# Kernel tuning notes

Hardware: AMD Instinct MI355X
Metric: run time of the kernel (lower is better)

## Reference

```python
import jax, jax.numpy as jnp
import numpy as np

N = 100000
E = 3200000
F_IN, HID, C = 256, 128, 40


def setup_inputs() -> dict:
    key = jax.random.key(0)
    k1, k2, k3, k4, k5 = jax.random.split(key, 5)
    x = jax.random.normal(k1, (N, F_IN), dtype=jnp.float32)
    edge_index = jax.random.randint(k2, (2, E), 0, N, dtype=jnp.int64)
    edge_weight = jax.random.uniform(k3, (E,), dtype=jnp.float32)
    W1 = jax.random.normal(k4, (F_IN, HID), dtype=jnp.float32) * (1.0 / np.sqrt(F_IN))
    b1 = jnp.zeros((HID,), dtype=jnp.float32)
    W2 = jax.random.normal(k5, (HID, C), dtype=jnp.float32) * (1.0 / np.sqrt(HID))
    b2 = jnp.zeros((C,), dtype=jnp.float32)
    return {"x": x, "edge_index": edge_index, "edge_weight": edge_weight,
            "W1": W1, "b1": b1, "W2": W2, "b2": b2}


def gcn_conv(x, edge_index, edge_weight, W, b):
    # PyG GCNConv (add_self_loops=False, normalize=False):
    # 1) linear transform, 2) edge-weighted scatter-add from src to dst.
    h = x @ W  # [N, d_out]
    src, dst = edge_index[0], edge_index[1]
    msgs = h[src] * edge_weight[:, None]  # [E, d_out]
    agg = jax.ops.segment_sum(msgs, dst, num_segments=x.shape[0])
    return agg + b


def reference(x, edge_index, edge_weight, W1, b1, W2, b2):
    # dropout is identity in eval mode
    h = jax.nn.relu(gcn_conv(x, edge_index, edge_weight, W1, b1))
    out = gcn_conv(h, edge_index, edge_weight, W2, b2)
    return jax.nn.log_softmax(out, axis=1)
```

## Files before the change

kernel.cpp:

```cpp
#include <hip/hip_runtime.h>
#include <hip/hip_bf16.h>
#include <hip/hip_fp16.h>
#include <math.h>

#define N_NODES 100000
#define E_EDGES 3200000
#define F_INF   256
#define HIDF    128
#define C_OUT   40

#define BSH   8
#define NB    391
#define NSEG  32
#define CAP   384
#define OCAP  262144
#define EPB   1563
#define SCAT_BLOCKS 2048
#define W1T_BLOCKS  128
#define GEMM1_BLOCKS ((N_NODES + 127) / 128)

typedef __attribute__((ext_vector_type(8))) short bf16x8;
typedef __attribute__((ext_vector_type(4))) float f32x4;

static __device__ __forceinline__ short bf16c(float f) {
    __hip_bfloat16 b = __float2bfloat16(f);
    return *reinterpret_cast<short*>(&b);
}

static __device__ void scat_body(int bid, const int* __restrict__ ei,
        const float* __restrict__ ew, int* __restrict__ cnt,
        int2* __restrict__ rec, int* __restrict__ ocnt,
        int2* __restrict__ osw, int* __restrict__ odst) {
    int seg = bid & (NSEG - 1);
    int e0 = bid * EPB;
    int e1 = e0 + EPB; if (e1 > E_EDGES) e1 = E_EDGES;
    for (int e = e0 + threadIdx.x; e < e1; e += 256) {
        int dst = ei[E_EDGES + e];
        int src = ei[e];
        float w = ew[e];
        int b = dst >> BSH;
        int packed = src | ((dst & 255) << 17);
        int pos = atomicAdd(&cnt[seg * NB + b], 1);
        if (pos < CAP) {
            rec[(size_t)(seg * NB + b) * CAP + pos] =
                make_int2(packed, __float_as_int(w));
        } else {
            int op = atomicAdd(ocnt, 1);
            if (op < OCAP) { osw[op] = make_int2(src, __float_as_int(w)); odst[op] = dst; }
        }
    }
}

static __device__ void w1t_body(int bid, const float* __restrict__ W1,
                                short* __restrict__ w1t) {
    int idx = bid * 256 + threadIdx.x;
    int k = idx >> 7, c = idx & 127;
    w1t[c * 256 + k] = bf16c(W1[idx]);
}

__global__ __launch_bounds__(256) void scat_w1t_kernel(const int* __restrict__ ei,
        const float* __restrict__ ew, int* __restrict__ cnt,
        int2* __restrict__ rec, int* __restrict__ ocnt,
        int2* __restrict__ osw, int* __restrict__ odst,
        const float* __restrict__ W1, short* __restrict__ w1t) {
    if (blockIdx.x < SCAT_BLOCKS)
        scat_body(blockIdx.x, ei, ew, cnt, rec, ocnt, osw, odst);
    else
        w1t_body(blockIdx.x - SCAT_BLOCKS, W1, w1t);
}

static __device__ void csr_body(char* smem, int b, const int* __restrict__ cnt,
        const int2* __restrict__ rec, const int* __restrict__ ocnt,
        const int2* __restrict__ osw, const int* __restrict__ odst,
        int* __restrict__ rowptr, int2* __restrict__ srcw) {
    int* hist = (int*)smem;
    int* sc   = hist + 256;
    int* cur  = sc + 256;
    int* red  = cur + 256;
    int* s_base = red + 4;
    int tid = threadIdx.x;
    hist[tid] = 0;

    int partial = 0;
    for (int i = tid; i < b * NSEG; i += 256) {
        int bp = i >> 5, s = i & 31;
        int c = cnt[s * NB + bp];
        partial += (c < CAP ? c : CAP);
    }
    int onum = *ocnt; if (onum > OCAP) onum = OCAP;
    for (int i = tid; i < onum; i += 256)
        if ((odst[i] >> BSH) < b) ++partial;
    #pragma unroll
    for (int off = 32; off; off >>= 1) partial += __shfl_xor(partial, off);
    if ((tid & 63) == 0) red[tid >> 6] = partial;
    __syncthreads();
    if (tid == 0) *s_base = red[0] + red[1] + red[2] + red[3];
    __syncthreads();

    for (int s = 0; s < NSEG; ++s) {
        int c = cnt[s * NB + b]; if (c > CAP) c = CAP;
        const int2* rp = &rec[(size_t)(s * NB + b) * CAP];
        for (int i = tid; i < c; i += 256)
            atomicAdd(&hist[(rp[i].x >> 17) & 255], 1);
    }
    for (int i = tid; i < onum; i += 256) {
        int d = odst[i];
        if ((d >> BSH) == b) atomicAdd(&hist[d & 255], 1);
    }
    __syncthreads();

    sc[tid] = hist[tid];
    __syncthreads();
    for (int off = 1; off < 256; off <<= 1) {
        int v = (tid >= off) ? sc[tid - off] : 0;
        __syncthreads();
        sc[tid] += v;
        __syncthreads();
    }
    int excl = (tid > 0) ? sc[tid - 1] : 0;
    cur[tid] = excl;
    int base = *s_base;
    int node = b * 256 + tid;
    if (node <= N_NODES) rowptr[node] = base + excl;
    __syncthreads();

    for (int s = 0; s < NSEG; ++s) {
        int c = cnt[s * NB + b]; if (c > CAP) c = CAP;
        const int2* rp = &rec[(size_t)(s * NB + b) * CAP];
        for (int i = tid; i < c; i += 256) {
            int2 r = rp[i];
            int dl = (r.x >> 17) & 255;
            int p = atomicAdd(&cur[dl], 1);
            srcw[base + p] = make_int2(r.x & 0x1FFFF, r.y);
        }
    }
    for (int i = tid; i < onum; i += 256) {
        int d = odst[i];
        if ((d >> BSH) == b) {
            int p = atomicAdd(&cur[d & 255], 1);
            srcw[base + p] = osw[i];
        }
    }
}

static __device__ void gemm1_body(char* smem, int bid, const float* __restrict__ x,
                                  const short* __restrict__ w1t,
                                  __half* __restrict__ h) {
    short* aT = (short*)smem;
    int tid = threadIdx.x;
    int lane = tid & 63, wid = tid >> 6;
    int wr = wid >> 1, wc = wid & 1;
    int m0 = bid * 128;
    f32x4 acc[4][4] = {{{0.f}}};
    for (int kb = 0; kb < 256; kb += 64) {
        #pragma unroll
        for (int t = 0; t < 8; ++t) {
            int id = tid + t * 256;
            int row = id >> 4, c4 = id & 15;
            int gr = m0 + row; if (gr >= N_NODES) gr = N_NODES - 1;
            float4 g = *(const float4*)&x[(size_t)gr * F_INF + kb + c4 * 4];
            short4 s4 = { bf16c(g.x), bf16c(g.y), bf16c(g.z), bf16c(g.w) };
            int byte = row * 128 + c4 * 8;
            byte ^= (row & 7) << 4;
            *(short4*)(smem + byte) = s4;
        }
        __syncthreads();
        #pragma unroll
        for (int km = 0; km < 2; ++km) {
            bf16x8 af[4], bfr[4];
            #pragma unroll
            for (int mi = 0; mi < 4; ++mi) {
                int row = wr * 64 + mi * 16 + (lane & 15);
                int kk = km * 32 + (lane >> 4) * 8;
                int byte = row * 128 + kk * 2;
                byte ^= (row & 7) << 4;
                af[mi] = *(bf16x8*)(smem + byte);
            }
            #pragma unroll
            for (int ni = 0; ni < 4; ++ni) {
                int col = wc * 64 + ni * 16 + (lane & 15);
                int kk = kb + km * 32 + (lane >> 4) * 8;
                bfr[ni] = *(const bf16x8*)&w1t[col * 256 + kk];
            }
            #pragma unroll
            for (int mi = 0; mi < 4; ++mi)
                #pragma unroll
                for (int ni = 0; ni < 4; ++ni)
                    acc[mi][ni] = __builtin_amdgcn_mfma_f32_16x16x32_bf16(
                        af[mi], bfr[ni], acc[mi][ni], 0, 0, 0);
        }
        __syncthreads();
    }
    #pragma unroll
    for (int mi = 0; mi < 4; ++mi) {
        int rbase = m0 + wr * 64 + mi * 16 + ((lane >> 4) << 2);
        #pragma unroll
        for (int ni = 0; ni < 4; ++ni) {
            int col = wc * 64 + ni * 16 + (lane & 15);
            #pragma unroll
            for (int r = 0; r < 4; ++r) {
                int row = rbase + r;
                if (row < N_NODES)
                    h[(size_t)row * HIDF + col] = __float2half(acc[mi][ni][r]);
            }
        }
    }
}

__global__ __launch_bounds__(256) void csr_gemm1_kernel(const int* __restrict__ cnt,
        const int2* __restrict__ rec, const int* __restrict__ ocnt,
        const int2* __restrict__ osw, const int* __restrict__ odst,
        int* __restrict__ rowptr, int2* __restrict__ srcw,
        const float* __restrict__ x, const short* __restrict__ w1t,
        __half* __restrict__ h) {
    __shared__ char smem[16384];
    if (blockIdx.x < NB)
        csr_body(smem, blockIdx.x, cnt, rec, ocnt, osw, odst, rowptr, srcw);
    else
        gemm1_body(smem, blockIdx.x - NB, x, w1t, h);
}

__global__ __launch_bounds__(256) void agg1_kernel(const __half* __restrict__ h,
                                                   const int2* __restrict__ srcw,
                                                   const int* __restrict__ rowptr,
                                                   const float* __restrict__ b1,
                                                   __half* __restrict__ hact) {
    int lane = threadIdx.x & 63;
    int node = blockIdx.x * 4 + (threadIdx.x >> 6);
    if (node >= N_NODES) return;
    int beg = rowptr[node], end = rowptr[node + 1];
    int eo = lane >> 4, fo = lane & 15;
    float4 a0 = {0.f, 0.f, 0.f, 0.f}, a1 = {0.f, 0.f, 0.f, 0.f};
    const uint4* hp = (const uint4*)h;
    for (int base = beg; base < end; base += 64) {
        int idx = base + lane;
        int2 sw = srcw[idx < end ? idx : end - 1];
        int cnt = end - base; if (cnt > 64) cnt = 64;
        for (int j = 0; j < cnt; j += 8) {
            int jj0 = j + eo, jj1 = j + 4 + eo;
            int s0 = __shfl(sw.x, jj0);
            float w0 = __int_as_float(__shfl(sw.y, jj0));
            int s1 = __shfl(sw.x, jj1);
            float w1 = __int_as_float(__shfl(sw.y, jj1));
            if (jj0 >= cnt) w0 = 0.f;
            if (jj1 >= cnt) w1 = 0.f;
            uint4 hv0 = hp[(size_t)s0 * 16 + fo];
            uint4 hv1 = hp[(size_t)s1 * 16 + fo];
            const __half2* p0 = (const __half2*)&hv0;
            const __half2* p1 = (const __half2*)&hv1;
            float2 f;
            f = __half22float2(p0[0]); a0.x += w0 * f.x; a0.y += w0 * f.y;
            f = __half22float2(p0[1]); a0.z += w0 * f.x; a0.w += w0 * f.y;
            f = __half22float2(p0[2]); a1.x += w0 * f.x; a1.y += w0 * f.y;
            f = __half22float2(p0[3]); a1.z += w0 * f.x; a1.w += w0 * f.y;
            f = __half22float2(p1[0]); a0.x += w1 * f.x; a0.y += w1 * f.y;
            f = __half22float2(p1[1]); a0.z += w1 * f.x; a0.w += w1 * f.y;
            f = __half22float2(p1[2]); a1.x += w1 * f.x; a1.y += w1 * f.y;
            f = __half22float2(p1[3]); a1.z += w1 * f.x; a1.w += w1 * f.y;
        }
    }
    #pragma unroll
    for (int off = 16; off < 64; off <<= 1) {
        a0.x += __shfl_xor(a0.x, off); a0.y += __shfl_xor(a0.y, off);
        a0.z += __shfl_xor(a0.z, off); a0.w += __shfl_xor(a0.w, off);
        a1.x += __shfl_xor(a1.x, off); a1.y += __shfl_xor(a1.y, off);
        a1.z += __shfl_xor(a1.z, off); a1.w += __shfl_xor(a1.w, off);
    }
    if (lane < 16) {
        float4 bb0 = *(const float4*)&b1[fo * 8];
        float4 bb1 = *(const float4*)&b1[fo * 8 + 4];
        __half2 o0 = __floats2half2_rn(fmaxf(a0.x + bb0.x, 0.f), fmaxf(a0.y + bb0.y, 0.f));
        __half2 o1 = __floats2half2_rn(fmaxf(a0.z + bb0.z, 0.f), fmaxf(a0.w + bb0.w, 0.f));
        __half2 o2 = __floats2half2_rn(fmaxf(a1.x + bb1.x, 0.f), fmaxf(a1.y + bb1.y, 0.f));
        __half2 o3 = __floats2half2_rn(fmaxf(a1.z + bb1.z, 0.f), fmaxf(a1.w + bb1.w, 0.f));
        uint4 ov = { *(uint*)&o0, *(uint*)&o1, *(uint*)&o2, *(uint*)&o3 };
        ((uint4*)hact)[(size_t)node * 16 + fo] = ov;
    }
}

__global__ __launch_bounds__(320) void gemm2_kernel(const __half* __restrict__ hact,
                                                    const float* __restrict__ W2,
                                                    __half* __restrict__ h2) {
    __shared__ float xT[128 * 68];
    __shared__ float w2[128 * 40];
    int tid = threadIdx.x;
    int tx = tid % 40, ty = tid / 40;
    int m0 = blockIdx.x * 64;
    for (int i = tid; i < 128 * 40; i += 320) w2[i] = W2[i];
    for (int i = tid; i < 1024; i += 320) {
        int row = i >> 4, c8 = i & 15;
        int gr = m0 + row; if (gr >= N_NODES) gr = N_NODES - 1;
        uint4 v = *(const uint4*)&hact[(size_t)gr * HIDF + c8 * 8];
        const __half2* ph = (const __half2*)&v;
        #pragma unroll
        for (int t = 0; t < 4; ++t) {
            float2 f = __half22float2(ph[t]);
            int k = c8 * 8 + t * 2;
            xT[(k + 0) * 68 + row] = f.x;
            xT[(k + 1) * 68 + row] = f.y;
        }
    }
    __syncthreads();
    float acc[8] = {};
    #pragma unroll 4
    for (int k = 0; k < 128; ++k) {
        float wv = w2[k * 40 + tx];
        float4 xa = *(float4*)&xT[k * 68 + ty * 8];
        float4 xb = *(float4*)&xT[k * 68 + ty * 8 + 4];
        acc[0] += xa.x * wv; acc[1] += xa.y * wv;
        acc[2] += xa.z * wv; acc[3] += xa.w * wv;
        acc[4] += xb.x * wv; acc[5] += xb.y * wv;
        acc[6] += xb.z * wv; acc[7] += xb.w * wv;
    }
    #pragma unroll
    for (int i = 0; i < 8; ++i) {
        int r = m0 + ty * 8 + i;
        if (r < N_NODES) h2[(size_t)r * C_OUT + tx] = __float2half(acc[i]);
    }
}

__global__ __launch_bounds__(256) void agg2_kernel(const __half* __restrict__ h2,
                                                   const int2* __restrict__ srcw,
                                                   const int* __restrict__ rowptr,
                                                   const float* __restrict__ b2,
                                                   float* __restrict__ out) {
    int lane = threadIdx.x & 63;
    int node = blockIdx.x * 4 + (threadIdx.x >> 6);
    if (node >= N_NODES) return;
    int beg = rowptr[node], end = rowptr[node + 1];
    int eo = lane >> 4, fo = lane & 15;
    float4 acc = {0.f, 0.f, 0.f, 0.f};
    const uint2* hp = (const uint2*)h2;
    for (int base = beg; base < end; base += 64) {
        int idx = base + lane;
        int2 sw = srcw[idx < end ? idx : end - 1];
        int cnt = end - base; if (cnt > 64) cnt = 64;
        for (int j = 0; j < cnt; j += 8) {
            int jj0 = j + eo, jj1 = j + 4 + eo;
            int s0 = __shfl(sw.x, jj0);
            float w0 = __int_as_float(__shfl(sw.y, jj0));
            int s1 = __shfl(sw.x, jj1);
            float w1 = __int_as_float(__shfl(sw.y, jj1));
            if (jj0 >= cnt) w0 = 0.f;
            if (jj1 >= cnt) w1 = 0.f;
            if (fo < 10) {
                uint2 hv0 = hp[(size_t)s0 * 10 + fo];
                uint2 hv1 = hp[(size_t)s1 * 10 + fo];
                float2 f;
                f = __half22float2(*(__half2*)&hv0.x); acc.x += w0 * f.x; acc.y += w0 * f.y;
                f = __half22float2(*(__half2*)&hv0.y); acc.z += w0 * f.x; acc.w += w0 * f.y;
                f = __half22float2(*(__half2*)&hv1.x); acc.x += w1 * f.x; acc.y += w1 * f.y;
                f = __half22float2(*(__half2*)&hv1.y); acc.z += w1 * f.x; acc.w += w1 * f.y;
            }
        }
    }
    #pragma unroll
    for (int off = 16; off < 64; off <<= 1) {
        acc.x += __shfl_xor(acc.x, off); acc.y += __shfl_xor(acc.y, off);
        acc.z += __shfl_xor(acc.z, off); acc.w += __shfl_xor(acc.w, off);
    }
    float4 v = {-INFINITY, -INFINITY, -INFINITY, -INFINITY};
    if (fo < 10) {
        float4 bb = *(const float4*)&b2[fo * 4];
        v.x = acc.x + bb.x; v.y = acc.y + bb.y;
        v.z = acc.z + bb.z; v.w = acc.w + bb.w;
    }
    float m = fmaxf(fmaxf(v.x, v.y), fmaxf(v.z, v.w));
    #pragma unroll
    for (int off = 8; off; off >>= 1) m = fmaxf(m, __shfl_xor(m, off));
    float ex = 0.f;
    if (fo < 10)
        ex = expf(v.x - m) + expf(v.y - m) + expf(v.z - m) + expf(v.w - m);
    #pragma unroll
    for (int off = 8; off; off >>= 1) ex += __shfl_xor(ex, off);
    float ls = logf(ex);
    if (lane < 16 && fo < 10) {
        float4 o = { v.x - m - ls, v.y - m - ls, v.z - m - ls, v.w - m - ls };
        *(float4*)&out[(size_t)node * C_OUT + fo * 4] = o;
    }
}


extern "C" void kernel_launch(void* const* d_in, const int* in_sizes, int n_in,
                              void* d_out, int out_size, void* d_ws, size_t ws_size,
                              hipStream_t stream) {
    const float* x  = (const float*)d_in[0];
    const int*   ei = (const int*)d_in[1];
    const float* ew = (const float*)d_in[2];
    const float* W1 = (const float*)d_in[3];
    const float* b1 = (const float*)d_in[4];
    const float* W2 = (const float*)d_in[5];
    const float* b2 = (const float*)d_in[6];
    float* out = (float*)d_out;

    char* ws = (char*)d_ws;
    size_t off = 0;
    auto alloc = [&](size_t bytes) -> void* {
        void* p = ws + off;
        off += (bytes + 255) & ~(size_t)255;
        return p;
    };
    __half* h      = (__half*)alloc((size_t)N_NODES * HIDF * 2);
    __half* hact   = (__half*)alloc((size_t)N_NODES * HIDF * 2);
    __half* h2     = (__half*)alloc((size_t)N_NODES * C_OUT * 2);
    short*  w1t    = (short*)alloc((size_t)HIDF * F_INF * 2);
    int*    rowptr = (int*)alloc((size_t)(N_NODES + 1) * 4);
    int2*   srcw   = (int2*)alloc((size_t)E_EDGES * 8);
    int2*   rec    = (int2*)alloc((size_t)NSEG * NB * CAP * 8);
    int*    cnt    = (int*)alloc((size_t)NSEG * NB * 4);
    int*    ocnt   = (int*)alloc(256);
    int2*   osw    = (int2*)alloc((size_t)OCAP * 8);
    int*    odst   = (int*)alloc((size_t)OCAP * 4);

    hipMemsetAsync(cnt, 0, (size_t)NSEG * NB * 4, stream);
    hipMemsetAsync(ocnt, 0, 4, stream);

    scat_w1t_kernel<<<SCAT_BLOCKS + W1T_BLOCKS, 256, 0, stream>>>(
        ei, ew, cnt, rec, ocnt, osw, odst, W1, w1t);
    csr_gemm1_kernel<<<NB + GEMM1_BLOCKS, 256, 0, stream>>>(
        cnt, rec, ocnt, osw, odst, rowptr, srcw, x, w1t, h);
    agg1_kernel<<<(N_NODES + 3) / 4, 256, 0, stream>>>(h, srcw, rowptr, b1, hact);
    gemm2_kernel<<<(N_NODES + 63) / 64, 320, 0, stream>>>(hact, W2, h2);
    agg2_kernel<<<(N_NODES + 3) / 4, 256, 0, stream>>>(h2, srcw, rowptr, b2, out);
}
```

Before: 559.5 us.

## Pad h2 to 64 halves and widen gather loads, prefetch edge lists

The layer-2 features are stored padded to 64 halfs per row (zero-filled tail) so agg2 can gather 16-byte rows with 8 lanes per edge and 8 edges in flight, replacing 8-byte loads with 10 of 16 lanes active. Both aggregation kernels now prefetch the next 64-edge chunk of src/weight records and issue four (agg1) or two (agg2) independent row gathers per iteration to raise memory-level parallelism. The padding adds extra h2 write and read traffic per row, and the larger unroll raises register pressure.

```diff
diff --git a/kernel.cpp b/kernel.cpp
--- a/kernel.cpp
+++ b/kernel.cpp
@@ -8,6 +8,7 @@
 #define F_INF   256
 #define HIDF    128
 #define C_OUT   40
+#define H2P     64
 
 #define BSH   8
 #define NB    391
@@ -146,7 +147,6 @@
 static __device__ void gemm1_body(char* smem, int bid, const float* __restrict__ x,
                                   const short* __restrict__ w1t,
                                   __half* __restrict__ h) {
-    short* aT = (short*)smem;
     int tid = threadIdx.x;
     int lane = tid & 63, wid = tid >> 6;
     int wr = wid >> 1, wc = wid & 1;
@@ -232,32 +232,35 @@
     int eo = lane >> 4, fo = lane & 15;
     float4 a0 = {0.f, 0.f, 0.f, 0.f}, a1 = {0.f, 0.f, 0.f, 0.f};
     const uint4* hp = (const uint4*)h;
+    int idx0 = beg + lane;
+    int2 sw = srcw[idx0 < end ? idx0 : end - 1];
     for (int base = beg; base < end; base += 64) {
-        int idx = base + lane;
-        int2 sw = srcw[idx < end ? idx : end - 1];
         int cnt = end - base; if (cnt > 64) cnt = 64;
-        for (int j = 0; j < cnt; j += 8) {
-            int jj0 = j + eo, jj1 = j + 4 + eo;
-            int s0 = __shfl(sw.x, jj0);
-            float w0 = __int_as_float(__shfl(sw.y, jj0));
-            int s1 = __shfl(sw.x, jj1);
-            float w1 = __int_as_float(__shfl(sw.y, jj1));
-            if (jj0 >= cnt) w0 = 0.f;
-            if (jj1 >= cnt) w1 = 0.f;
-            uint4 hv0 = hp[(size_t)s0 * 16 + fo];
-            uint4 hv1 = hp[(size_t)s1 * 16 + fo];
-            const __half2* p0 = (const __half2*)&hv0;
-            const __half2* p1 = (const __half2*)&hv1;
-            float2 f;
-            f = __half22float2(p0[0]); a0.x += w0 * f.x; a0.y += w0 * f.y;
-            f = __half22float2(p0[1]); a0.z += w0 * f.x; a0.w += w0 * f.y;
-            f = __half22float2(p0[2]); a1.x += w0 * f.x; a1.y += w0 * f.y;
-            f = __half22float2(p0[3]); a1.z += w0 * f.x; a1.w += w0 * f.y;
-            f = __half22float2(p1[0]); a0.x += w1 * f.x; a0.y += w1 * f.y;
-            f = __half22float2(p1[1]); a0.z += w1 * f.x; a0.w += w1 * f.y;
-            f = __half22float2(p1[2]); a1.x += w1 * f.x; a1.y += w1 * f.y;
-            f = __half22float2(p1[3]); a1.z += w1 * f.x; a1.w += w1 * f.y;
-        }
+        int nidx = base + 64 + lane;
+        int2 swn = srcw[nidx < end ? nidx : end - 1];
+        for (int j = 0; j < cnt; j += 16) {
+            int s[4]; float w[4];
+            #pragma unroll
+            for (int u = 0; u < 4; ++u) {
+                int jj = j + u * 4 + eo;
+                s[u] = __shfl(sw.x, jj);
+                w[u] = __int_as_float(__shfl(sw.y, jj));
+                if (jj >= cnt) w[u] = 0.f;
+            }
+            uint4 hv[4];
+            #pragma unroll
+            for (int u = 0; u < 4; ++u) hv[u] = hp[(size_t)s[u] * 16 + fo];
+            #pragma unroll
+            for (int u = 0; u < 4; ++u) {
+                const __half2* p = (const __half2*)&hv[u];
+                float2 f;
+                f = __half22float2(p[0]); a0.x += w[u] * f.x; a0.y += w[u] * f.y;
+                f = __half22float2(p[1]); a0.z += w[u] * f.x; a0.w += w[u] * f.y;
+                f = __half22float2(p[2]); a1.x += w[u] * f.x; a1.y += w[u] * f.y;
+                f = __half22float2(p[3]); a1.z += w[u] * f.x; a1.w += w[u] * f.y;
+            }
+        }
+        sw = swn;
     }
     #pragma unroll
     for (int off = 16; off < 64; off <<= 1) {
@@ -280,7 +283,7 @@
 
 __global__ __launch_bounds__(320) void gemm2_kernel(const __half* __restrict__ hact,
                                                     const float* __restrict__ W2,
-                                                    __half* __restrict__ h2) {
+                                                    __half* __restrict__ h2p) {
     __shared__ float xT[128 * 68];
     __shared__ float w2[128 * 40];
     int tid = threadIdx.x;
@@ -300,6 +303,14 @@
             xT[(k + 1) * 68 + row] = f.y;
         }
     }
+    for (int i = tid; i < 64 * 3; i += 320) {
+        int row = i / 3, c = i % 3;
+        int gr = m0 + row;
+        if (gr < N_NODES) {
+            uint4 z = {0, 0, 0, 0};
+            *(uint4*)&h2p[(size_t)gr * H2P + 40 + c * 8] = z;
+        }
+    }
     __syncthreads();
     float acc[8] = {};
     #pragma unroll 4
@@ -315,11 +326,11 @@
     #pragma unroll
     for (int i = 0; i < 8; ++i) {
         int r = m0 + ty * 8 + i;
-        if (r < N_NODES) h2[(size_t)r * C_OUT + tx] = __float2half(acc[i]);
-    }
-}
-
-__global__ __launch_bounds__(256) void agg2_kernel(const __half* __restrict__ h2,
+        if (r < N_NODES) h2p[(size_t)r * H2P + tx] = __float2half(acc[i]);
+    }
+}
+
+__global__ __launch_bounds__(256) void agg2_kernel(const __half* __restrict__ h2p,
                                                    const int2* __restrict__ srcw,
                                                    const int* __restrict__ rowptr,
                                                    const float* __restrict__ b2,
@@ -328,55 +339,76 @@
     int node = blockIdx.x * 4 + (threadIdx.x >> 6);
     if (node >= N_NODES) return;
     int beg = rowptr[node], end = rowptr[node + 1];
-    int eo = lane >> 4, fo = lane & 15;
-    float4 acc = {0.f, 0.f, 0.f, 0.f};
-    const uint2* hp = (const uint2*)h2;
+    int eo = lane >> 3, fo = lane & 7;
+    float4 a0 = {0.f, 0.f, 0.f, 0.f}, a1 = {0.f, 0.f, 0.f, 0.f};
+    const uint4* hp = (const uint4*)h2p;
+    int idx0 = beg + lane;
+    int2 sw = srcw[idx0 < end ? idx0 : end - 1];
     for (int base = beg; base < end; base += 64) {
-        int idx = base + lane;
-        int2 sw = srcw[idx < end ? idx : end - 1];
         int cnt = end - base; if (cnt > 64) cnt = 64;
-        for (int j = 0; j < cnt; j += 8) {
-            int jj0 = j + eo, jj1 = j + 4 + eo;
-            int s0 = __shfl(sw.x, jj0);
-            float w0 = __int_as_float(__shfl(sw.y, jj0));
-            int s1 = __shfl(sw.x, jj1);
-            float w1 = __int_as_float(__shfl(sw.y, jj1));
-            if (jj0 >= cnt) w0 = 0.f;
-            if (jj1 >= cnt) w1 = 0.f;
-            if (fo < 10) {
-                uint2 hv0 = hp[(size_t)s0 * 10 + fo];
-                uint2 hv1 = hp[(size_t)s1 * 10 + fo];
+        int nidx = base + 64 + lane;
+        int2 swn = srcw[nidx < end ? nidx : end - 1];
+        for (int j = 0; j < cnt; j += 16) {
+            int s[2]; float w[2];
+            #pragma unroll
+            for (int u = 0; u < 2; ++u) {
+                int jj = j + u * 8 + eo;
+                s[u] = __shfl(sw.x, jj);
+                w[u] = __int_as_float(__shfl(sw.y, jj));
+                if (jj >= cnt) w[u] = 0.f;
+            }
+            uint4 hv[2];
+            #pragma unroll
+            for (int u = 0; u < 2; ++u) hv[u] = hp[(size_t)s[u] * 8 + fo];
+            #pragma unroll
+            for (int u = 0; u < 2; ++u) {
+                const __half2* p = (const __half2*)&hv[u];
                 float2 f;
-                f = __half22float2(*(__half2*)&hv0.x); acc.x += w0 * f.x; acc.y += w0 * f.y;
-                f = __half22float2(*(__half2*)&hv0.y); acc.z += w0 * f.x; acc.w += w0 * f.y;
-                f = __half22float2(*(__half2*)&hv1.x); acc.x += w1 * f.x; acc.y += w1 * f.y;
-                f = __half22float2(*(__half2*)&hv1.y); acc.z += w1 * f.x; acc.w += w1 * f.y;
-            }
-        }
-    }
-    #pragma unroll
-    for (int off = 16; off < 64; off <<= 1) {
-        acc.x += __shfl_xor(acc.x, off); acc.y += __shfl_xor(acc.y, off);
-        acc.z += __shfl_xor(acc.z, off); acc.w += __shfl_xor(acc.w, off);
-    }
-    float4 v = {-INFINITY, -INFINITY, -INFINITY, -INFINITY};
-    if (fo < 10) {
-        float4 bb = *(const float4*)&b2[fo * 4];
-        v.x = acc.x + bb.x; v.y = acc.y + bb.y;
-        v.z = acc.z + bb.z; v.w = acc.w + bb.w;
-    }
-    float m = fmaxf(fmaxf(v.x, v.y), fmaxf(v.z, v.w));
-    #pragma unroll
-    for (int off = 8; off; off >>= 1) m = fmaxf(m, __shfl_xor(m, off));
+                f = __half22float2(p[0]); a0.x += w[u] * f.x; a0.y += w[u] * f.y;
+                f = __half22float2(p[1]); a0.z += w[u] * f.x; a0.w += w[u] * f.y;
+                f = __half22float2(p[2]); a1.x += w[u] * f.x; a1.y += w[u] * f.y;
+                f = __half22float2(p[3]); a1.z += w[u] * f.x; a1.w += w[u] * f.y;
+            }
+        }
+        sw = swn;
+    }
+    #pragma unroll
+    for (int off = 8; off < 64; off <<= 1) {
+        a0.x += __shfl_xor(a0.x, off); a0.y += __shfl_xor(a0.y, off);
+        a0.z += __shfl_xor(a0.z, off); a0.w += __shfl_xor(a0.w, off);
+        a1.x += __shfl_xor(a1.x, off); a1.y += __shfl_xor(a1.y, off);
+        a1.z += __shfl_xor(a1.z, off); a1.w += __shfl_xor(a1.w, off);
+    }
+    float v[8];
+    bool act = (lane < 8) && (fo < 5);
+    #pragma unroll
+    for (int t = 0; t < 8; ++t) v[t] = -INFINITY;
+    if (act) {
+        float4 bb0 = *(const float4*)&b2[fo * 8];
+        float4 bb1 = *(const float4*)&b2[fo * 8 + 4];
+        v[0] = a0.x + bb0.x; v[1] = a0.y + bb0.y;
+        v[2] = a0.z + bb0.z; v[3] = a0.w + bb0.w;
+        v[4] = a1.x + bb1.x; v[5] = a1.y + bb1.y;
+        v[6] = a1.z + bb1.z; v[7] = a1.w + bb1.w;
+    }
+    float m = v[0];
+    #pragma unroll
+    for (int t = 1; t < 8; ++t) m = fmaxf(m, v[t]);
+    #pragma unroll
+    for (int off = 1; off < 8; off <<= 1) m = fmaxf(m, __shfl_xor(m, off));
     float ex = 0.f;
-    if (fo < 10)
-        ex = expf(v.x - m) + expf(v.y - m) + expf(v.z - m) + expf(v.w - m);
-    #pragma unroll
-    for (int off = 8; off; off >>= 1) ex += __shfl_xor(ex, off);
+    if (act) {
+        #pragma unroll
+        for (int t = 0; t < 8; ++t) ex += expf(v[t] - m);
+    }
+    #pragma unroll
+    for (int off = 1; off < 8; off <<= 1) ex += __shfl_xor(ex, off);
     float ls = logf(ex);
-    if (lane < 16 && fo < 10) {
-        float4 o = { v.x - m - ls, v.y - m - ls, v.z - m - ls, v.w - m - ls };
-        *(float4*)&out[(size_t)node * C_OUT + fo * 4] = o;
+    if (act) {
+        float4 o0 = { v[0]-m-ls, v[1]-m-ls, v[2]-m-ls, v[3]-m-ls };
+        float4 o1 = { v[4]-m-ls, v[5]-m-ls, v[6]-m-ls, v[7]-m-ls };
+        *(float4*)&out[(size_t)node * C_OUT + fo * 8] = o0;
+        *(float4*)&out[(size_t)node * C_OUT + fo * 8 + 4] = o1;
     }
 }
 
@@ -402,7 +434,7 @@
     };
     __half* h      = (__half*)alloc((size_t)N_NODES * HIDF * 2);
     __half* hact   = (__half*)alloc((size_t)N_NODES * HIDF * 2);
-    __half* h2     = (__half*)alloc((size_t)N_NODES * C_OUT * 2);
+    __half* h2p    = (__half*)alloc((size_t)N_NODES * H2P * 2);
     short*  w1t    = (short*)alloc((size_t)HIDF * F_INF * 2);
     int*    rowptr = (int*)alloc((size_t)(N_NODES + 1) * 4);
     int2*   srcw   = (int2*)alloc((size_t)E_EDGES * 8);
@@ -420,6 +452,6 @@
     csr_gemm1_kernel<<<NB + GEMM1_BLOCKS, 256, 0, stream>>>(
         cnt, rec, ocnt, osw, odst, rowptr, srcw, x, w1t, h);
     agg1_kernel<<<(N_NODES + 3) / 4, 256, 0, stream>>>(h, srcw, rowptr, b1, hact);
-    gemm2_kernel<<<(N_NODES + 63) / 64, 320, 0, stream>>>(hact, W2, h2);
-    agg2_kernel<<<(N_NODES + 3) / 4, 256, 0, stream>>>(h2, srcw, rowptr, b2, out);
-}
+    gemm2_kernel<<<(N_NODES + 63) / 64, 320, 0, stream>>>(hact, W2, h2p);
+    agg2_kernel<<<(N_NODES + 3) / 4, 256, 0, stream>>>(h2p, srcw, rowptr, b2, out);
+}
```

After: 548.4 us. 2.0% less time.
